# Kernel tuning notes

Measured on AMD Instinct MI355X. Metric: run time of the kernel, lower is better.

## Reference

```python
import jax, jax.numpy as jnp
import numpy as np

EPS = 1.0    # Lennard-Jones well depth
SIGMA = 1.0  # Lennard-Jones length scale


def setup_inputs() -> dict:
    key = jax.random.key(0)
    k1, k2, k3, k4 = jax.random.split(key, 4)
    B, N, D = 2, 4096, 3
    q = jax.random.normal(k1, (B, N, D), dtype=jnp.float32)
    p = jax.random.normal(k2, (B, N, D), dtype=jnp.float32)
    # masses strictly positive, away from zero
    m = jax.random.uniform(k3, (B, N, 1), dtype=jnp.float32, minval=0.5, maxval=1.5)
    t = jax.random.uniform(k4, (), dtype=jnp.float32)
    return {"q": q, "p": p, "m": m, "t": t}


def _lj_pair_force(q):
    # disp[b,i,j,:] = q[b,i,:] - q[b,j,:]   (torch: unsqueeze(-2) - unsqueeze(-3))
    disp = q[..., :, None, :] - q[..., None, :, :]          # [B,N,N,3]
    r2 = jnp.sum(disp * disp, axis=-1)                      # [B,N,N]
    mask = r2 > 0.0                                          # excludes i==j diagonal
    safe_r2 = jnp.where(mask, r2, 1.0)
    inv_r2 = jnp.where(mask, 1.0 / safe_r2, 0.0)
    s2 = (SIGMA * SIGMA) * inv_r2
    s6 = s2 * s2 * s2
    # LJ force on i from j: 24*eps*(2*s12 - s6)/r^2 * disp
    coeff = 24.0 * EPS * inv_r2 * s6 * (2.0 * s6 - 1.0)      # [B,N,N]
    force = coeff[..., None] * disp                          # [B,N,N,3]
    # sum(axis=-2): sum over partner index j
    return jnp.sum(force, axis=-2)                           # [B,N,3]


def reference(q, p, m, t):
    dq = p / m                   # Experiment.dq
    dp = _lj_pair_force(q)       # BasePairPotential.dp with LJ force
    return (dq, dp)
```

## Files before the change

kernel.cpp:

```cpp
#include <hip/hip_runtime.h>

#define BATCH    2
#define NPART    4096
#define NTHREADS 256
#define IBLK     4
#define ILANES   2
#define JCH      (NTHREADS / ILANES)
#define JLEN     (NPART / JCH)
#define NIB      (NPART / IBLK)
#define NWAVES   (NTHREADS / 64)

typedef float v2f __attribute__((ext_vector_type(2)));

template <bool MASKED>
__device__ inline void lj_body(float jx, float jy, float jz,
                               v2f qx, v2f qy, v2f qz,
                               v2f& fx, v2f& fy, v2f& fz) {
    const v2f dx = qx - (v2f)jx;
    const v2f dy = qy - (v2f)jy;
    const v2f dz = qz - (v2f)jz;
    v2f r2 = dx * dx;
    r2 = __builtin_elementwise_fma(dy, dy, r2);
    r2 = __builtin_elementwise_fma(dz, dz, r2);
    v2f inv;
    if (MASKED) {
        inv.x = (r2.x > 0.0f) ? __builtin_amdgcn_rcpf(r2.x) : 0.0f;
        inv.y = (r2.y > 0.0f) ? __builtin_amdgcn_rcpf(r2.y) : 0.0f;
    } else {
        inv.x = __builtin_amdgcn_rcpf(r2.x);
        inv.y = __builtin_amdgcn_rcpf(r2.y);
    }
    const v2f inv2 = inv * inv;
    const v2f s6 = inv2 * inv;
    const v2f c1 = __builtin_elementwise_fma((v2f)48.0f, s6, (v2f)(-24.0f));
    const v2f coeff = (inv * s6) * c1;
    fx = __builtin_elementwise_fma(coeff, dx, fx);
    fy = __builtin_elementwise_fma(coeff, dy, fy);
    fz = __builtin_elementwise_fma(coeff, dz, fz);
}

template <bool MASKED>
__device__ inline void chunk_loop(const float4* __restrict__ jq4,
                                  v2f qx, v2f qy, v2f qz,
                                  v2f& fx, v2f& fy, v2f& fz) {
    #pragma unroll 2
    for (int it = 0; it < JLEN / 4; ++it) {
        const float4 A = jq4[3 * it + 0];
        const float4 B = jq4[3 * it + 1];
        const float4 C = jq4[3 * it + 2];
        lj_body<MASKED>(A.x, A.y, A.z, qx, qy, qz, fx, fy, fz);
        lj_body<MASKED>(A.w, B.x, B.y, qx, qy, qz, fx, fy, fz);
        lj_body<MASKED>(B.z, B.w, C.x, qx, qy, qz, fx, fy, fz);
        lj_body<MASKED>(C.y, C.z, C.w, qx, qy, qz, fx, fy, fz);
    }
}

__global__ __launch_bounds__(NTHREADS, 8) void lj_fused(
        const float* __restrict__ q, const float* __restrict__ p,
        const float* __restrict__ m, float* __restrict__ dq,
        float* __restrict__ dp) {
    __shared__ float red2[NWAVES * 12];

    const int ib = blockIdx.x;
    const int b  = blockIdx.y;
    const int t  = threadIdx.x;
    const int il = t & 1;
    const int jc = t >> 1;

    const float* qb = q + (size_t)b * NPART * 3;

    const int i0 = ib * IBLK + il;
    const int i1 = i0 + ILANES;
    const v2f qx = {qb[i0 * 3 + 0], qb[i1 * 3 + 0]};
    const v2f qy = {qb[i0 * 3 + 1], qb[i1 * 3 + 1]};
    const v2f qz = {qb[i0 * 3 + 2], qb[i1 * 3 + 2]};

    v2f fx = (v2f)0.0f, fy = (v2f)0.0f, fz = (v2f)0.0f;

    const float4* jq4 = (const float4*)(qb + (size_t)jc * JLEN * 3);

    const int diagc = ib >> 3;
    if (__any(jc == diagc)) {
        chunk_loop<true >(jq4, qx, qy, qz, fx, fy, fz);
    } else {
        chunk_loop<false>(jq4, qx, qy, qz, fx, fy, fz);
    }

    #pragma unroll
    for (int msk = 2; msk <= 32; msk <<= 1) {
        fx.x += __shfl_xor(fx.x, msk); fx.y += __shfl_xor(fx.y, msk);
        fy.x += __shfl_xor(fy.x, msk); fy.y += __shfl_xor(fy.y, msk);
        fz.x += __shfl_xor(fz.x, msk); fz.y += __shfl_xor(fz.y, msk);
    }
    const int w    = t >> 6;
    const int lane = t & 63;
    if (lane < 2) {
        float* r = &red2[w * 12 + lane * 6];
        r[0] = fx.x; r[1] = fx.y;
        r[2] = fy.x; r[3] = fy.y;
        r[4] = fz.x; r[5] = fz.y;
    }
    __syncthreads();

    if (t < 12) {
        const int c   = t >> 2;
        const int ii  = t & 3;
        const int h   = ii >> 1;
        const int il2 = ii & 1;
        const int slot = il2 * 6 + c * 2 + h;
        float s = 0.0f;
        #pragma unroll
        for (int wv = 0; wv < NWAVES; ++wv) s += red2[wv * 12 + slot];
        const size_t gi = (size_t)b * NPART + ib * IBLK + ii;
        dp[gi * 3 + c] = s;
        dq[gi * 3 + c] = p[gi * 3 + c] / m[gi];
    }
}

extern "C" void kernel_launch(void* const* d_in, const int* in_sizes, int n_in,
                              void* d_out, int out_size, void* d_ws, size_t ws_size,
                              hipStream_t stream) {
    const float* q = (const float*)d_in[0];
    const float* p = (const float*)d_in[1];
    const float* m = (const float*)d_in[2];

    const int n_elem = BATCH * NPART * 3;
    float* dq_out = (float*)d_out;
    float* dp_out = (float*)d_out + n_elem;

    dim3 grid(NIB, BATCH);
    lj_fused<<<grid, NTHREADS, 0, stream>>>(q, p, m, dq_out, dp_out);
}
```

Baseline: 21.11 us.

## Double i-block per workgroup and reduce partial forces through shared memory

Workgroups now have 512 threads, each covering 8 target particles with 4 i-lanes. Every j coordinate loaded from cache is therefore reused across twice as many i particles, and the grid is half as large. The cross-wave shuffle reduction is replaced by a two-stage reduction through shared memory, and the j loop is fully unrolled. The larger block and the unchanged occupancy bound of 8 per CU may put pressure on registers, and the extra LDS traffic and barriers add some overhead.

```diff
diff --git a/kernel.cpp b/kernel.cpp
--- a/kernel.cpp
+++ b/kernel.cpp
@@ -2,13 +2,12 @@
 
 #define BATCH    2
 #define NPART    4096
-#define NTHREADS 256
-#define IBLK     4
-#define ILANES   2
+#define NTHREADS 512
+#define IBLK     8
+#define ILANES   4
 #define JCH      (NTHREADS / ILANES)
 #define JLEN     (NPART / JCH)
 #define NIB      (NPART / IBLK)
-#define NWAVES   (NTHREADS / 64)
 
 typedef float v2f __attribute__((ext_vector_type(2)));
 
@@ -43,7 +42,7 @@
 __device__ inline void chunk_loop(const float4* __restrict__ jq4,
                                   v2f qx, v2f qy, v2f qz,
                                   v2f& fx, v2f& fy, v2f& fz) {
-    #pragma unroll 2
+    #pragma unroll
     for (int it = 0; it < JLEN / 4; ++it) {
         const float4 A = jq4[3 * it + 0];
         const float4 B = jq4[3 * it + 1];
@@ -59,13 +58,14 @@
         const float* __restrict__ q, const float* __restrict__ p,
         const float* __restrict__ m, float* __restrict__ dq,
         float* __restrict__ dp) {
-    __shared__ float red2[NWAVES * 12];
+    __shared__ float red[JCH * 6 * ILANES];
+    __shared__ float red2[24 * 8];
 
     const int ib = blockIdx.x;
     const int b  = blockIdx.y;
     const int t  = threadIdx.x;
-    const int il = t & 1;
-    const int jc = t >> 1;
+    const int il = t & (ILANES - 1);
+    const int jc = t >> 2;
 
     const float* qb = q + (size_t)b * NPART * 3;
 
@@ -79,38 +79,43 @@
 
     const float4* jq4 = (const float4*)(qb + (size_t)jc * JLEN * 3);
 
-    const int diagc = ib >> 3;
-    if (__any(jc == diagc)) {
+    if ((t >> 6) == (ib >> 6)) {
         chunk_loop<true >(jq4, qx, qy, qz, fx, fy, fz);
     } else {
         chunk_loop<false>(jq4, qx, qy, qz, fx, fy, fz);
     }
 
-    #pragma unroll
-    for (int msk = 2; msk <= 32; msk <<= 1) {
-        fx.x += __shfl_xor(fx.x, msk); fx.y += __shfl_xor(fx.y, msk);
-        fy.x += __shfl_xor(fy.x, msk); fy.y += __shfl_xor(fy.y, msk);
-        fz.x += __shfl_xor(fz.x, msk); fz.y += __shfl_xor(fz.y, msk);
-    }
-    const int w    = t >> 6;
-    const int lane = t & 63;
-    if (lane < 2) {
-        float* r = &red2[w * 12 + lane * 6];
-        r[0] = fx.x; r[1] = fx.y;
-        r[2] = fy.x; r[3] = fy.y;
-        r[4] = fz.x; r[5] = fz.y;
+    red[(jc * 6 + 0) * ILANES + il] = fx.x;
+    red[(jc * 6 + 1) * ILANES + il] = fx.y;
+    red[(jc * 6 + 2) * ILANES + il] = fy.x;
+    red[(jc * 6 + 3) * ILANES + il] = fy.y;
+    red[(jc * 6 + 4) * ILANES + il] = fz.x;
+    red[(jc * 6 + 5) * ILANES + il] = fz.y;
+    __syncthreads();
+
+    if (t < 192) {
+        const int sl = t >> 3;
+        const int g  = t & 7;
+        const int slot = sl >> 2;
+        const int il2  = sl & 3;
+        float s = 0.0f;
+        #pragma unroll
+        for (int qq = 0; qq < 16; ++qq) {
+            s += red[((g * 16 + qq) * 6 + slot) * ILANES + il2];
+        }
+        red2[sl * 8 + g] = s;
     }
     __syncthreads();
 
-    if (t < 12) {
-        const int c   = t >> 2;
-        const int ii  = t & 3;
-        const int h   = ii >> 1;
-        const int il2 = ii & 1;
-        const int slot = il2 * 6 + c * 2 + h;
+    if (t < 24) {
         float s = 0.0f;
         #pragma unroll
-        for (int wv = 0; wv < NWAVES; ++wv) s += red2[wv * 12 + slot];
+        for (int g = 0; g < 8; ++g) s += red2[t * 8 + g];
+        const int slot = t >> 2;
+        const int il2  = t & 3;
+        const int c  = slot >> 1;
+        const int h  = slot & 1;
+        const int ii = h * ILANES + il2;
         const size_t gi = (size_t)b * NPART + ib * IBLK + ii;
         dp[gi * 3 + c] = s;
         dq[gi * 3 + c] = p[gi * 3 + c] / m[gi];
```

After: 17.52 us, median of 2. -17.0%, faster.
